# Optimization experiments

Hardware: AMD Instinct MI355X
Metric: run time of the kernel (lower is better)

## Reference

```python
import jax, jax.numpy as jnp
import numpy as np
import math

D_MODEL = 32
N_HEADS = 2
FEAT_DIM = 16
HEAD_DIM = 16  # d_model // num_key_value_heads
EPS = 1e-12
R2 = math.sqrt(2.0)
RD = math.sqrt(FEAT_DIM)
RRD = math.sqrt(RD)


def taylor_exp(x):
    # x: (b, h, l, f) -> (b, h, l, 1 + f + f*f)
    b, h, l, f = x.shape
    x2 = (x[..., :, None] * x[..., None, :]).reshape(b, h, l, f * f) / R2
    term1 = jnp.ones_like(x[..., :1])
    term2 = x / RRD
    term3 = x2 / RD
    return jnp.concatenate([term1, term2, term3], axis=-1)


def setup_inputs() -> dict:
    key = jax.random.key(0)
    ks = jax.random.split(key, 5)
    b, l = 4, 2048
    return {
        "hidden_states": jax.random.normal(ks[0], (b, l, D_MODEL), dtype=jnp.float32),
        "Wq": jax.random.normal(ks[1], (FEAT_DIM * N_HEADS, D_MODEL), dtype=jnp.float32) * (1.0 / math.sqrt(D_MODEL)),
        "Wk": jax.random.normal(ks[2], (FEAT_DIM * N_HEADS, D_MODEL), dtype=jnp.float32) * (1.0 / math.sqrt(D_MODEL)),
        "Wv": jax.random.normal(ks[3], (N_HEADS * HEAD_DIM, D_MODEL), dtype=jnp.float32) * (1.0 / math.sqrt(D_MODEL)),
        "Wo": jax.random.normal(ks[4], (D_MODEL, N_HEADS * HEAD_DIM), dtype=jnp.float32) * (1.0 / math.sqrt(D_MODEL)),
    }


def reference(hidden_states, Wq, Wk, Wv, Wo):
    b, l, _ = hidden_states.shape
    # projections (nn.Linear: x @ W.T)
    q = (hidden_states @ Wq.T).reshape(b, l, N_HEADS, FEAT_DIM).transpose(0, 2, 1, 3)  # (b,h,l,f)
    k = (hidden_states @ Wk.T).reshape(b, l, N_HEADS, FEAT_DIM).transpose(0, 2, 1, 3)
    v = (hidden_states @ Wv.T).reshape(b, l, N_HEADS, HEAD_DIM).transpose(0, 2, 1, 3)  # (b,h,l,d)

    q = taylor_exp(q)  # (b,h,l,D) with D = 1+f+f^2 = 273
    k = taylor_exp(k)

    # causal linear attention: num_t = q_t . sum_{s<=t} k_s v_s^T
    kv = jnp.cumsum(k[..., None, :] * v[..., :, None], axis=2)  # (b,h,l,d,D)
    num = jnp.einsum('bhlD,bhldD->bhld', q, kv)                  # (b,h,l,d)
    denom = jnp.einsum('bhlD,bhlD->bhl', q, jnp.cumsum(k, axis=2)) + EPS
    y = num / denom[..., None]

    y = y.transpose(0, 2, 1, 3).reshape(b, l, N_HEADS * HEAD_DIM)  # (b,l,h*d)
    return (y @ Wo.T).astype(hidden_states.dtype)
```

## Files before the change

kernel.cpp:

```cpp
#include <hip/hip_runtime.h>
#include <hip/hip_fp16.h>
#include <math.h>

#define B 4
#define H 2
#define L 2048
#define DM 32
#define F 16
#define HD 16
#define DD 273
#define DDP 280
#define CHK 64
#define NC (L / CHK)
#define BH (B * H)

#define SC_LIN 0.5f
#define SC_QUAD 0.17677669529663687f

__global__ __launch_bounds__(256) void chunksum_kernel(
    const float* __restrict__ hs, const float* __restrict__ Wq,
    const float* __restrict__ Wk, const float* __restrict__ Wv,
    float* __restrict__ qp, float* __restrict__ kp, float* __restrict__ vp,
    float* __restrict__ S_kv, float* __restrict__ S_k) {
  int blk = blockIdx.x;
  int bh = blk >> 5, ch = blk & (NC - 1);
  int b = bh >> 1, h = bh & 1;
  int lane = threadIdx.x & 63, wave = threadIdx.x >> 6;
  int l = ch * CHK + lane;

  __shared__ float ks[CHK][F + 1];
  __shared__ __half vs_h[CHK][F];

  float x[DM];
  const float4* xr = (const float4*)(hs + ((size_t)b * L + l) * DM);
#pragma unroll
  for (int j = 0; j < DM / 4; j++) {
    float4 v = xr[j];
    x[4 * j] = v.x; x[4 * j + 1] = v.y; x[4 * j + 2] = v.z; x[4 * j + 3] = v.w;
  }
  for (int c = wave * 12; c < wave * 12 + 12; c++) {
    int kind = c >> 4;
    int f = c & 15;
    const float* __restrict__ W = (kind == 0) ? Wq : (kind == 1) ? Wk : Wv;
    const float* wr = W + (size_t)(h * 16 + f) * DM;
    float acc = 0.f;
#pragma unroll
    for (int i = 0; i < DM; i++) acc += x[i] * wr[i];
    float* dst = (kind == 0) ? qp : (kind == 1) ? kp : vp;
    dst[((size_t)bh * L + l) * F + f] = acc;
    if (kind == 1) ks[lane][f] = acc;
    if (kind == 2) vs_h[lane][f] = __float2half(acc);
  }
  if (threadIdx.x < CHK) ks[threadIdx.x][16] = 1.0f;
  __syncthreads();

#pragma unroll
  for (int rep = 0; rep < 2; rep++) {
    int dd = threadIdx.x + rep * 256;
    if (dd >= DDP) break;
    float* dst = S_kv + ((size_t)blk * DDP + dd) * HD;
    if (dd >= DD) {
#pragma unroll
      for (int hh = 0; hh < HD; hh++) dst[hh] = 0.f;
      S_k[(size_t)blk * DDP + dd] = 0.f;
      continue;
    }
    int i, j;
    float sc;
    if (dd == 0) {
      i = 16; j = 16; sc = 1.0f;
    } else if (dd <= F) {
      i = dd - 1; j = 16; sc = SC_LIN;
    } else {
      int m = dd - 17;
      i = m >> 4; j = m & 15; sc = SC_QUAD;
    }
    float acc[HD];
#pragma unroll
    for (int hh = 0; hh < HD; hh++) acc[hh] = 0.f;
    float acck = 0.f;
    for (int p = 0; p < CHK; p++) {
      float kf = sc * ks[p][i] * ks[p][j];
      acck += kf;
      const __half2* vr = (const __half2*)vs_h[p];
#pragma unroll
      for (int x2 = 0; x2 < 8; x2++) {
        float2 vf = __half22float2(vr[x2]);
        acc[2 * x2] += kf * vf.x;
        acc[2 * x2 + 1] += kf * vf.y;
      }
    }
#pragma unroll
    for (int hh = 0; hh < HD; hh++) dst[hh] = acc[hh];
    S_k[(size_t)blk * DDP + dd] = acck;
  }
}

#define PSLICES 19
__global__ __launch_bounds__(256) void prefix_kernel(float* __restrict__ S_kv,
                                                     float* __restrict__ S_k) {
  int blk = blockIdx.x;
  int bh = blk / PSLICES, sl = blk % PSLICES;
  int e = sl * 256 + threadIdx.x;
  if (e < DDP * HD) {
    size_t base = (size_t)bh * NC * DDP * HD + e;
    float v[NC];
#pragma unroll
    for (int c = 0; c < NC; c++) v[c] = S_kv[base + (size_t)c * DDP * HD];
    float run = 0.f;
#pragma unroll
    for (int c = 0; c < NC; c++) {
      S_kv[base + (size_t)c * DDP * HD] = run;
      run += v[c];
    }
  } else if (e < DDP * HD + DDP) {
    int e2 = e - DDP * HD;
    size_t base = (size_t)bh * NC * DDP + e2;
    float v[NC];
#pragma unroll
    for (int c = 0; c < NC; c++) v[c] = S_k[base + (size_t)c * DDP];
    float run = 0.f;
#pragma unroll
    for (int c = 0; c < NC; c++) {
      S_k[base + (size_t)c * DDP] = run;
      run += v[c];
    }
  }
}

__global__ __launch_bounds__(512) void outchunk_kernel(
    const float* __restrict__ qp, const float* __restrict__ kp,
    const float* __restrict__ vp, const float* __restrict__ St_kv,
    const float* __restrict__ St_k, float* __restrict__ y) {
  int blk = blockIdx.x;
  int bh = blk >> 5, ch = blk & (NC - 1);
  int b = bh >> 1, h = bh & 1;
  int t = threadIdx.x & 63;
  int u = __builtin_amdgcn_readfirstlane(threadIdx.x >> 6);

  __shared__ float qs[CHK][F + 1];
  __shared__ float red[8][CHK][21];

  if (threadIdx.x < 256) {
    const float4* qb =
        (const float4*)(qp + ((size_t)bh * L + (size_t)ch * CHK) * F);
    int r = threadIdx.x >> 2, c4 = (threadIdx.x & 3) * 4;
    float4 v = qb[threadIdx.x];
    qs[r][c4] = v.x; qs[r][c4 + 1] = v.y; qs[r][c4 + 2] = v.z; qs[r][c4 + 3] = v.w;
    if (threadIdx.x < CHK) qs[threadIdx.x][16] = 1.0f;
  }

  float qreg[F];
  const float4* qrow =
      (const float4*)(qp + ((size_t)bh * L + (size_t)ch * CHK + t) * F);
#pragma unroll
  for (int j = 0; j < 4; j++) {
    float4 v = qrow[j];
    qreg[4 * j] = v.x; qreg[4 * j + 1] = v.y;
    qreg[4 * j + 2] = v.z; qreg[4 * j + 3] = v.w;
  }
  __syncthreads();

  float acc[HD];
#pragma unroll
  for (int hh = 0; hh < HD; hh++) acc[hh] = 0.f;
  float den = 0.f;

  const float* __restrict__ Sbase = St_kv + (size_t)blk * DDP * HD;
  const float* __restrict__ Skb = St_k + (size_t)blk * DDP;

#pragma unroll 5
  for (int m = 0; m < 35; m++) {
    int dd = u + (m << 3);
    float phi;
    if (dd == 0) {
      phi = 1.0f;
    } else if (dd <= F) {
      phi = qs[t][dd - 1] * SC_LIN;
    } else {
      int mm = dd - 17;
      phi = qs[t][mm >> 4] * qs[t][mm & 15] * SC_QUAD;
    }
    phi = (dd < DD) ? phi : 0.0f;
    den += phi * Skb[dd];
    const float4* Sr = (const float4*)(Sbase + dd * HD);
    float4 s0 = Sr[0], s1 = Sr[1], s2 = Sr[2], s3 = Sr[3];
    acc[0] += phi * s0.x;  acc[1] += phi * s0.y;
    acc[2] += phi * s0.z;  acc[3] += phi * s0.w;
    acc[4] += phi * s1.x;  acc[5] += phi * s1.y;
    acc[6] += phi * s1.z;  acc[7] += phi * s1.w;
    acc[8] += phi * s2.x;  acc[9] += phi * s2.y;
    acc[10] += phi * s2.z; acc[11] += phi * s2.w;
    acc[12] += phi * s3.x; acc[13] += phi * s3.y;
    acc[14] += phi * s3.z; acc[15] += phi * s3.w;
  }

  const float* __restrict__ kbase = kp + ((size_t)bh * L + (size_t)ch * CHK) * F;
  const float* __restrict__ vbase = vp + ((size_t)bh * L + (size_t)ch * CHK) * F;
#pragma unroll
  for (int mm = 0; mm < CHK / 8; mm++) {
    int s = u + mm * 8;
    const float4* kr = (const float4*)(kbase + s * F);
    float4 k0 = kr[0], k1 = kr[1], k2 = kr[2], k3 = kr[3];
    float dot = qreg[0] * k0.x + qreg[1] * k0.y + qreg[2] * k0.z +
                qreg[3] * k0.w + qreg[4] * k1.x + qreg[5] * k1.y +
                qreg[6] * k1.z + qreg[7] * k1.w + qreg[8] * k2.x +
                qreg[9] * k2.y + qreg[10] * k2.z + qreg[11] * k2.w +
                qreg[12] * k3.x + qreg[13] * k3.y + qreg[14] * k3.z +
                qreg[15] * k3.w;
    float scv = 1.0f + dot * 0.25f + dot * dot * 0.03125f;
    scv = (s <= t) ? scv : 0.0f;
    den += scv;
    const float4* vr = (const float4*)(vbase + s * F);
    float4 v0 = vr[0], v1 = vr[1], v2 = vr[2], v3 = vr[3];
    acc[0] += scv * v0.x;  acc[1] += scv * v0.y;
    acc[2] += scv * v0.z;  acc[3] += scv * v0.w;
    acc[4] += scv * v1.x;  acc[5] += scv * v1.y;
    acc[6] += scv * v1.z;  acc[7] += scv * v1.w;
    acc[8] += scv * v2.x;  acc[9] += scv * v2.y;
    acc[10] += scv * v2.z; acc[11] += scv * v2.w;
    acc[12] += scv * v3.x; acc[13] += scv * v3.y;
    acc[14] += scv * v3.z; acc[15] += scv * v3.w;
  }

#pragma unroll
  for (int hh = 0; hh < HD; hh++) red[u][t][hh] = acc[hh];
  red[u][t][16] = den;
  __syncthreads();

  for (int idx = threadIdx.x; idx < CHK * 17; idx += 512) {
    int t2 = idx / 17, e = idx % 17;
    float sum = 0.f;
#pragma unroll
    for (int w = 0; w < 8; w++) sum += red[w][t2][e];
    red[0][t2][e] = sum;
  }
  __syncthreads();

  if (threadIdx.x < CHK) {
    int t2 = threadIdx.x;
    float inv = 1.0f / (red[0][t2][16] + 1e-12f);
    float* yb = y + (((size_t)(b * L + ch * CHK + t2)) * H + h) * HD;
#pragma unroll
    for (int hh = 0; hh < HD; hh++) yb[hh] = red[0][t2][hh] * inv;
  }
}

__global__ __launch_bounds__(256) void out_kernel(const float* __restrict__ y,
                                                  const float* __restrict__ Wo,
                                                  float* __restrict__ out) {
  int lane = threadIdx.x & 63;
  int wave = __builtin_amdgcn_readfirstlane(threadIdx.x >> 6);
  int row = blockIdx.x * 64 + lane;
  float yr[DM];
  const float4* yb = (const float4*)(y + (size_t)row * DM);
#pragma unroll
  for (int j = 0; j < DM / 4; j++) {
    float4 v = yb[j];
    yr[4 * j] = v.x; yr[4 * j + 1] = v.y; yr[4 * j + 2] = v.z; yr[4 * j + 3] = v.w;
  }
  for (int c = wave * 8; c < wave * 8 + 8; c++) {
    const float* __restrict__ wr = Wo + (size_t)c * DM;
    float acc = 0.f;
#pragma unroll
    for (int i = 0; i < DM; i++) acc += yr[i] * wr[i];
    out[(size_t)row * DM + c] = acc;
  }
}

extern "C" void kernel_launch(void* const* d_in, const int* in_sizes, int n_in,
                              void* d_out, int out_size, void* d_ws,
                              size_t ws_size, hipStream_t stream) {
  const float* hs = (const float*)d_in[0];
  const float* Wq = (const float*)d_in[1];
  const float* Wk = (const float*)d_in[2];
  const float* Wv = (const float*)d_in[3];
  const float* Wo = (const float*)d_in[4];
  float* out = (float*)d_out;

  float* ws = (float*)d_ws;
  float* qp = ws;
  float* kp = qp + (size_t)BH * L * F;
  float* vp = kp + (size_t)BH * L * F;
  float* S_kv = vp + (size_t)BH * L * F;
  float* S_k = S_kv + (size_t)BH * NC * DDP * HD;
  float* y = S_k + (size_t)BH * NC * DDP;

  chunksum_kernel<<<BH * NC, 256, 0, stream>>>(hs, Wq, Wk, Wv, qp, kp, vp,
                                               S_kv, S_k);
  prefix_kernel<<<BH * PSLICES, 256, 0, stream>>>(S_kv, S_k);
  outchunk_kernel<<<BH * NC, 512, 0, stream>>>(qp, kp, vp, S_kv, S_k, y);
  out_kernel<<<B * L / 64, 256, 0, stream>>>(y, Wo, out);
}
```

Measured before the change: 108.2 us.

## Split chunk-sum work into half-chunks per block and merge halves in prefix

The chunk-sum kernel now launches two blocks per 64-row chunk, each covering 32 rows, so there are twice as many blocks and each thread runs half as many serial iterations. Each block writes its partial state into a separate half of a doubled S buffer. The prefix kernel adds the two halves while scanning and writes into new P buffers. V is read as fp32 float4 from global memory instead of being staged as fp16 in shared memory. This buys more parallelism and better fp32 accuracy, at the cost of twice the partial-state write traffic and more global loads in the inner loop.

```diff
diff --git a/kernel.cpp b/kernel.cpp
--- a/kernel.cpp
+++ b/kernel.cpp
@@ -1,5 +1,4 @@
 #include <hip/hip_runtime.h>
-#include <hip/hip_fp16.h>
 #include <math.h>
 
 #define B 4
@@ -13,6 +12,7 @@
 #define CHK 64
 #define NC (L / CHK)
 #define BH (B * H)
+#define HCHK 32
 
 #define SC_LIN 0.5f
 #define SC_QUAD 0.17677669529663687f
@@ -23,14 +23,16 @@
     float* __restrict__ qp, float* __restrict__ kp, float* __restrict__ vp,
     float* __restrict__ S_kv, float* __restrict__ S_k) {
   int blk = blockIdx.x;
-  int bh = blk >> 5, ch = blk & (NC - 1);
+  int half = blk & 1;
+  int bc = blk >> 1;
+  int bh = bc >> 5, ch = bc & (NC - 1);
   int b = bh >> 1, h = bh & 1;
-  int lane = threadIdx.x & 63, wave = threadIdx.x >> 6;
-  int l = ch * CHK + lane;
-
-  __shared__ float ks[CHK][F + 1];
-  __shared__ __half vs_h[CHK][F];
-
+
+  __shared__ float ks[HCHK][F + 1];
+
+  int r = threadIdx.x & 31;
+  int g = threadIdx.x >> 5;
+  int l = ch * CHK + half * HCHK + r;
   float x[DM];
   const float4* xr = (const float4*)(hs + ((size_t)b * L + l) * DM);
 #pragma unroll
@@ -38,7 +40,9 @@
     float4 v = xr[j];
     x[4 * j] = v.x; x[4 * j + 1] = v.y; x[4 * j + 2] = v.z; x[4 * j + 3] = v.w;
   }
-  for (int c = wave * 12; c < wave * 12 + 12; c++) {
+#pragma unroll
+  for (int q = 0; q < 6; q++) {
+    int c = g * 6 + q;
     int kind = c >> 4;
     int f = c & 15;
     const float* __restrict__ W = (kind == 0) ? Wq : (kind == 1) ? Wk : Wv;
@@ -48,21 +52,24 @@
     for (int i = 0; i < DM; i++) acc += x[i] * wr[i];
     float* dst = (kind == 0) ? qp : (kind == 1) ? kp : vp;
     dst[((size_t)bh * L + l) * F + f] = acc;
-    if (kind == 1) ks[lane][f] = acc;
-    if (kind == 2) vs_h[lane][f] = __float2half(acc);
-  }
-  if (threadIdx.x < CHK) ks[threadIdx.x][16] = 1.0f;
+    if (kind == 1) ks[r][f] = acc;
+  }
+  if (threadIdx.x < HCHK) ks[threadIdx.x][16] = 1.0f;
   __syncthreads();
+
+  const float* __restrict__ vbase =
+      vp + ((size_t)bh * L + (size_t)ch * CHK + half * HCHK) * F;
+  size_t sblk = (size_t)half * (BH * NC) + bc;
 
 #pragma unroll
   for (int rep = 0; rep < 2; rep++) {
     int dd = threadIdx.x + rep * 256;
     if (dd >= DDP) break;
-    float* dst = S_kv + ((size_t)blk * DDP + dd) * HD;
+    float* dst = S_kv + (sblk * DDP + dd) * HD;
     if (dd >= DD) {
 #pragma unroll
       for (int hh = 0; hh < HD; hh++) dst[hh] = 0.f;
-      S_k[(size_t)blk * DDP + dd] = 0.f;
+      S_k[sblk * DDP + dd] = 0.f;
       continue;
     }
     int i, j;
@@ -79,51 +86,55 @@
 #pragma unroll
     for (int hh = 0; hh < HD; hh++) acc[hh] = 0.f;
     float acck = 0.f;
-    for (int p = 0; p < CHK; p++) {
+    for (int p = 0; p < HCHK; p++) {
       float kf = sc * ks[p][i] * ks[p][j];
       acck += kf;
-      const __half2* vr = (const __half2*)vs_h[p];
-#pragma unroll
-      for (int x2 = 0; x2 < 8; x2++) {
-        float2 vf = __half22float2(vr[x2]);
-        acc[2 * x2] += kf * vf.x;
-        acc[2 * x2 + 1] += kf * vf.y;
-      }
+      const float4* vr = (const float4*)(vbase + p * F);
+      float4 v0 = vr[0], v1 = vr[1], v2 = vr[2], v3 = vr[3];
+      acc[0] += kf * v0.x;  acc[1] += kf * v0.y;
+      acc[2] += kf * v0.z;  acc[3] += kf * v0.w;
+      acc[4] += kf * v1.x;  acc[5] += kf * v1.y;
+      acc[6] += kf * v1.z;  acc[7] += kf * v1.w;
+      acc[8] += kf * v2.x;  acc[9] += kf * v2.y;
+      acc[10] += kf * v2.z; acc[11] += kf * v2.w;
+      acc[12] += kf * v3.x; acc[13] += kf * v3.y;
+      acc[14] += kf * v3.z; acc[15] += kf * v3.w;
     }
 #pragma unroll
     for (int hh = 0; hh < HD; hh++) dst[hh] = acc[hh];
-    S_k[(size_t)blk * DDP + dd] = acck;
+    S_k[sblk * DDP + dd] = acck;
   }
 }
 
 #define PSLICES 19
-__global__ __launch_bounds__(256) void prefix_kernel(float* __restrict__ S_kv,
-                                                     float* __restrict__ S_k) {
+__global__ __launch_bounds__(256) void prefix_kernel(
+    const float* __restrict__ S_kv, const float* __restrict__ S_k,
+    float* __restrict__ P_kv, float* __restrict__ P_k) {
   int blk = blockIdx.x;
   int bh = blk / PSLICES, sl = blk % PSLICES;
   int e = sl * 256 + threadIdx.x;
+  const size_t HS_KV = (size_t)BH * NC * DDP * HD;
+  const size_t HS_K = (size_t)BH * NC * DDP;
   if (e < DDP * HD) {
     size_t base = (size_t)bh * NC * DDP * HD + e;
-    float v[NC];
-#pragma unroll
-    for (int c = 0; c < NC; c++) v[c] = S_kv[base + (size_t)c * DDP * HD];
     float run = 0.f;
 #pragma unroll
     for (int c = 0; c < NC; c++) {
-      S_kv[base + (size_t)c * DDP * HD] = run;
-      run += v[c];
+      size_t idx = base + (size_t)c * DDP * HD;
+      float v = S_kv[idx] + S_kv[idx + HS_KV];
+      P_kv[idx] = run;
+      run += v;
     }
   } else if (e < DDP * HD + DDP) {
     int e2 = e - DDP * HD;
     size_t base = (size_t)bh * NC * DDP + e2;
-    float v[NC];
-#pragma unroll
-    for (int c = 0; c < NC; c++) v[c] = S_k[base + (size_t)c * DDP];
     float run = 0.f;
 #pragma unroll
     for (int c = 0; c < NC; c++) {
-      S_k[base + (size_t)c * DDP] = run;
-      run += v[c];
+      size_t idx = base + (size_t)c * DDP;
+      float v = S_k[idx] + S_k[idx + HS_K];
+      P_k[idx] = run;
+      run += v;
     }
   }
 }
@@ -146,7 +157,8 @@
         (const float4*)(qp + ((size_t)bh * L + (size_t)ch * CHK) * F);
     int r = threadIdx.x >> 2, c4 = (threadIdx.x & 3) * 4;
     float4 v = qb[threadIdx.x];
-    qs[r][c4] = v.x; qs[r][c4 + 1] = v.y; qs[r][c4 + 2] = v.z; qs[r][c4 + 3] = v.w;
+    qs[r][c4] = v.x; qs[r][c4 + 1] = v.y;
+    qs[r][c4 + 2] = v.z; qs[r][c4 + 3] = v.w;
     if (threadIdx.x < CHK) qs[threadIdx.x][16] = 1.0f;
   }
 
@@ -283,12 +295,14 @@
   float* kp = qp + (size_t)BH * L * F;
   float* vp = kp + (size_t)BH * L * F;
   float* S_kv = vp + (size_t)BH * L * F;
-  float* S_k = S_kv + (size_t)BH * NC * DDP * HD;
-  float* y = S_k + (size_t)BH * NC * DDP;
-
-  chunksum_kernel<<<BH * NC, 256, 0, stream>>>(hs, Wq, Wk, Wv, qp, kp, vp,
-                                               S_kv, S_k);
-  prefix_kernel<<<BH * PSLICES, 256, 0, stream>>>(S_kv, S_k);
-  outchunk_kernel<<<BH * NC, 512, 0, stream>>>(qp, kp, vp, S_kv, S_k, y);
+  float* S_k = S_kv + (size_t)2 * BH * NC * DDP * HD;
+  float* P_kv = S_k + (size_t)2 * BH * NC * DDP;
+  float* P_k = P_kv + (size_t)BH * NC * DDP * HD;
+  float* y = P_k + (size_t)BH * NC * DDP;
+
+  chunksum_kernel<<<BH * NC * 2, 256, 0, stream>>>(hs, Wq, Wk, Wv, qp, kp, vp,
+                                                   S_kv, S_k);
+  prefix_kernel<<<BH * PSLICES, 256, 0, stream>>>(S_kv, S_k, P_kv, P_k);
+  outchunk_kernel<<<BH * NC, 512, 0, stream>>>(qp, kp, vp, P_kv, P_k, y);
   out_kernel<<<B * L / 64, 256, 0, stream>>>(y, Wo, out);
 }
```

Result: no change. 108.9 us (+0.7%).
